# Kernel tuning notes

Hardware: AMD Instinct MI355X
Metric: run time of the kernel (lower is better)

Reference implementation:

```python
import jax, jax.numpy as jnp
import numpy as np

OUT_SIZE = 14
CUTOFF = 0.2
VAR0 = 4            # var[0], mixin_factor = 0.0 -> current std = var[0]
BETA = 4.0
N_SQ = OUT_SIZE * OUT_SIZE
TAU = 0.5 / N_SQ
BATCH = 256
CHANNELS = 512


def _gkern_np(kernlen, std, vmin, vmax):
    n = np.arange(kernlen) - (kernlen - 1) / 2.0
    w = np.exp(-(n ** 2) / (2.0 * std * std))
    g = np.outer(w, w)
    return g * (vmax - vmin) + vmin


def _build_templates():
    n = OUT_SIZE
    base = _gkern_np(2 * n - 1, VAR0, -CUTOFF, 1.0)
    base = np.maximum(base, 0.0) * 2.0 - 1.0
    base = TAU * np.clip(BETA * base / n, -1.0, None)  # clamp(min=-1) only
    # unfold(0,n,1).unfold(1,n,1).reshape(-1,n,n) == sliding windows, row-major
    t = np.lib.stride_tricks.sliding_window_view(base, (n, n)).reshape(-1, n, n)
    t = np.flip(t, axis=0).copy()  # torch.flip(templates, dims=(0,))
    templates_f = jnp.asarray(t, jnp.float32)                    # (n^2, n, n)
    neg = -TAU * jnp.ones((1, n, n), jnp.float32)
    templates_b = jnp.concatenate([templates_f, neg], axis=0)    # (n^2+1, n, n)
    alpha = N_SQ / (1.0 + N_SQ)
    p_T = jnp.asarray(
        np.array([alpha / N_SQ] * N_SQ + [1.0 - alpha], np.float32))  # (n^2+1,)
    return templates_f, templates_b, p_T


def setup_inputs() -> dict:
    key = jax.random.key(0)
    templates_f, templates_b, p_T = _build_templates()
    x = jax.random.normal(key, (BATCH, CHANNELS, OUT_SIZE, OUT_SIZE), jnp.float32)
    return {"x": x, "templates_f": templates_f,
            "templates_b": templates_b, "p_T": p_T}


def reference(x, templates_f, templates_b, p_T):
    B, C, H, W = x.shape
    tau = 0.5 / (H * W)
    # max_pool2d with kernel == full spatial extent -> flat argmax per (b, c)
    idx = jnp.argmax(x.reshape(B, C, H * W), axis=-1)            # (B, C) int
    sel = templates_f[idx]                                       # (B, C, H, W)
    mask = sel / jnp.max(sel)                                    # global max
    mask = jax.nn.relu(mask - CUTOFF) / CUTOFF
    x_masked = x * mask
    # local loss (mutual-information style) on the masked activations
    tr_x_T = jnp.einsum('bcwh,twh->cbt', x_masked * tau, templates_b)  # (C,B,T)
    p_x_T = jax.nn.softmax(tr_x_T, axis=1)                       # softmax over b
    p_x = jnp.einsum('t,cbt->cb', p_T, p_x_T)                    # (C, B)
    log_ratio = jnp.log(p_x_T / p_x[:, :, None])                 # (C, B, T)
    p_x_T_log = jnp.einsum('cbt,cbt->ct', p_x_T, log_ratio)      # (C, T)
    loss = -jnp.einsum('t,ct->c', p_T, p_x_T_log)                # (C,)
    return x_masked, mask, loss
```

## Files before the change

kernel.cpp:

```cpp
#include <hip/hip_runtime.h>

#define BB 256
#define CCH 512
#define HW 196
#define TT 197
#define TROWS 208
#define NFRAG (13 * 7)
#define ASHORTS (NFRAG * 64 * 8)
#define H1FRAG (7 * 7)
#define H2FRAG (6 * 7)
#define H1SHORTS (H1FRAG * 512)
#define H2SHORTS (H2FRAG * 512)

typedef __attribute__((ext_vector_type(8))) short bf16x8;
typedef __attribute__((ext_vector_type(4))) float f32x4;

__device__ __forceinline__ unsigned short f2bf(float f) {
    union { float f; unsigned u; } v; v.f = f;
    unsigned r = v.u + 0x7FFFu + ((v.u >> 16) & 1u);
    return (unsigned short)(r >> 16);
}

__global__ void prep(const float* __restrict__ tf, const float* __restrict__ tb,
                     float* __restrict__ wsf, unsigned short* __restrict__ tb_bf) {
    if (blockIdx.x < 182) {
        int i = blockIdx.x * 256 + threadIdx.x;
        int frag = i >> 9;
        int s    = i & 511;
        int mt = frag / 7, kt = frag % 7;
        int lane = s >> 3, j = s & 7;
        int r = mt * 16 + (lane & 15);
        int k = kt * 32 + (lane >> 4) * 8 + j;
        const float tau = 0.5f / 196.0f;
        float v = (r < TT && k < HW) ? tb[r * HW + k] * tau : 0.0f;
        tb_bf[i] = f2bf(v);
    } else {
        __shared__ float red[256];
        float m = -1e30f;
        for (int i = threadIdx.x; i < HW * HW; i += 256) m = fmaxf(m, tf[i]);
        red[threadIdx.x] = m;
        __syncthreads();
        for (int s = 128; s > 0; s >>= 1) {
            if (threadIdx.x < s) red[threadIdx.x] = fmaxf(red[threadIdx.x], red[threadIdx.x + s]);
            __syncthreads();
        }
        if (threadIdx.x == 0) wsf[0] = red[0];
    }
}

extern "C" __global__ __launch_bounds__(1024)
void fused_one(const float* __restrict__ x, const float* __restrict__ tf,
               const float* __restrict__ pT, const unsigned short* __restrict__ tb_bf,
               const float* __restrict__ wsf,
               float* __restrict__ xm_out, float* __restrict__ mask_out,
               float* __restrict__ loss_out)
{
    extern __shared__ char smem[];
    unsigned short* Alds = (unsigned short*)smem;
    float* s_part = (float*)(smem + H1SHORTS * 2);
    float* rAs    = s_part + 16 * TROWS;
    float* pTs    = rAs + TROWS;
    float* red    = pTs + TROWS;

    const int c    = blockIdx.x;
    const int tid  = threadIdx.x;
    const int lane = tid & 63;
    const int w    = tid >> 6;
    const int l15  = lane & 15, lg = lane >> 4;
    const float rg = 1.0f / wsf[0];

    {
        const f32x4* src = (const f32x4*)tb_bf;
        f32x4* dst = (f32x4*)Alds;
        #pragma unroll
        for (int it = 0; it < 4; ++it) {
            int idx = tid + it * 1024;
            if (idx < H1SHORTS / 8) dst[idx] = src[idx];
        }
    }
    if (tid < TROWS) pTs[tid] = (tid < TT) ? pT[tid] : 0.0f;

    const int b = w * 16 + l15;
    const size_t rowoff = ((size_t)b * CCH + c) * HW;
    const float* xrow = x + rowoff;

    f32x4 u[13];
    #pragma unroll
    for (int kt = 0; kt < 6; ++kt) {
        u[2 * kt]     = *(const f32x4*)(xrow + kt * 32 + lg * 8);
        u[2 * kt + 1] = *(const f32x4*)(xrow + kt * 32 + lg * 8 + 4);
    }
    if (lg == 0) u[12] = *(const f32x4*)(xrow + 192);
    else         u[12] = (f32x4){-__builtin_inff(), -__builtin_inff(),
                                 -__builtin_inff(), -__builtin_inff()};

    float bv = -__builtin_inff(); int bi = 0;
    #pragma unroll
    for (int j = 0; j < 13; ++j) {
        const int k0 = (j < 12) ? (((j >> 1) * 8 + lg * 2 + (j & 1)) * 4) : 192;
        #pragma unroll
        for (int e = 0; e < 4; ++e) {
            float v = u[j][e];
            if (v > bv) { bv = v; bi = k0 + e; }
        }
    }
    #pragma unroll
    for (int m = 16; m <= 32; m <<= 1) {
        float ov = __shfl_xor(bv, m, 64);
        int   oi = __shfl_xor(bi, m, 64);
        if (ov > bv || (ov == bv && oi < bi)) { bv = ov; bi = oi; }
    }

    const float* selrow = tf + (size_t)bi * HW;
    float* xmrow = xm_out + rowoff;
    float* mkrow = mask_out + rowoff;
    bf16x8 fr[7];

    #pragma unroll
    for (int kt = 0; kt < 6; ++kt) {
        #pragma unroll
        for (int h = 0; h < 2; ++h) {
            const int k0 = kt * 32 + lg * 8 + h * 4;
            f32x4 sel = *(const f32x4*)(selrow + k0);
            f32x4 mk, xm;
            #pragma unroll
            for (int e = 0; e < 4; ++e) {
                float m = fmaxf(sel[e] * rg - 0.2f, 0.0f) * 5.0f;
                mk[e] = m;
                xm[e] = u[2 * kt + h][e] * m;
            }
            *(f32x4*)(xmrow + k0) = xm;
            *(f32x4*)(mkrow + k0) = mk;
            #pragma unroll
            for (int e = 0; e < 4; ++e) fr[kt][h * 4 + e] = (short)f2bf(xm[e]);
        }
    }
    {
        fr[6] = (bf16x8){0, 0, 0, 0, 0, 0, 0, 0};
        if (lg == 0) {
            f32x4 sel = *(const f32x4*)(selrow + 192);
            f32x4 mk, xm;
            #pragma unroll
            for (int e = 0; e < 4; ++e) {
                float m = fmaxf(sel[e] * rg - 0.2f, 0.0f) * 5.0f;
                mk[e] = m;
                xm[e] = u[12][e] * m;
            }
            *(f32x4*)(xmrow + 192) = xm;
            *(f32x4*)(mkrow + 192) = mk;
            #pragma unroll
            for (int e = 0; e < 4; ++e) fr[6][e] = (short)f2bf(xm[e]);
        }
    }

    __syncthreads();

    f32x4 acc[13];
    #pragma unroll
    for (int mt = 0; mt < 13; ++mt) acc[mt] = (f32x4){0.f, 0.f, 0.f, 0.f};

    const unsigned short* Abase = Alds + lane * 8;
    #pragma unroll
    for (int kt = 0; kt < 7; ++kt) {
        const bf16x8 bfrag = fr[kt];
        #pragma unroll
        for (int mt = 0; mt < 7; ++mt) {
            bf16x8 afrag = *(const bf16x8*)(Abase + (mt * 7 + kt) * 512);
            acc[mt] = __builtin_amdgcn_mfma_f32_16x16x32_bf16(afrag, bfrag, acc[mt], 0, 0, 0);
        }
    }

    __syncthreads();

    {
        const f32x4* src = (const f32x4*)(tb_bf + H1SHORTS);
        f32x4* dst = (f32x4*)Alds;
        #pragma unroll
        for (int it = 0; it < 3; ++it) {
            int idx = tid + it * 1024;
            if (idx < H2SHORTS / 8) dst[idx] = src[idx];
        }
    }
    __syncthreads();

    #pragma unroll
    for (int kt = 0; kt < 7; ++kt) {
        const bf16x8 bfrag = fr[kt];
        #pragma unroll
        for (int mt = 7; mt < 13; ++mt) {
            bf16x8 afrag = *(const bf16x8*)(Abase + ((mt - 7) * 7 + kt) * 512);
            acc[mt] = __builtin_amdgcn_mfma_f32_16x16x32_bf16(afrag, bfrag, acc[mt], 0, 0, 0);
        }
    }

    float* sp = s_part + w * TROWS;
    #pragma unroll
    for (int mt = 0; mt < 13; ++mt) {
        #pragma unroll
        for (int e = 0; e < 4; ++e) acc[mt][e] = __expf(acc[mt][e]);
        f32x4 s = acc[mt];
        #pragma unroll
        for (int m = 1; m <= 8; m <<= 1) {
            #pragma unroll
            for (int e = 0; e < 4; ++e) s[e] += __shfl_xor(s[e], m, 64);
        }
        if (l15 == 0) *(f32x4*)(sp + mt * 16 + lg * 4) = s;
    }
    __syncthreads();
    if (tid < TROWS) {
        float s = 0.f;
        #pragma unroll
        for (int w2 = 0; w2 < 16; ++w2) s += s_part[w2 * TROWS + tid];
        rAs[tid] = 1.0f / s;
    }
    __syncthreads();

    float px = 0.f;
    #pragma unroll
    for (int mt = 0; mt < 13; ++mt) {
        const int t0 = mt * 16 + lg * 4;
        f32x4 ra = *(const f32x4*)(rAs + t0);
        f32x4 pt = *(const f32x4*)(pTs + t0);
        #pragma unroll
        for (int e = 0; e < 4; ++e) {
            float p = acc[mt][e] * ra[e];
            acc[mt][e] = p;
            px += pt[e] * p;
        }
    }
    px += __shfl_xor(px, 16, 64);
    px += __shfl_xor(px, 32, 64);
    const float rpx = 1.0f / px;

    float part = 0.f;
    #pragma unroll
    for (int mt = 0; mt < 13; ++mt) {
        const int t0 = mt * 16 + lg * 4;
        f32x4 pt = *(const f32x4*)(pTs + t0);
        #pragma unroll
        for (int e = 0; e < 4; ++e) {
            float p = acc[mt][e];
            part += pt[e] * p * __logf(p * rpx);
        }
    }
    #pragma unroll
    for (int off = 32; off >= 1; off >>= 1) part += __shfl_xor(part, off, 64);
    if (lane == 0) red[w] = part;
    __syncthreads();
    if (tid == 0) {
        float s = 0.f;
        #pragma unroll
        for (int w2 = 0; w2 < 16; ++w2) s += red[w2];
        loss_out[c] = -s;
    }
}

extern "C" void kernel_launch(void* const* d_in, const int* in_sizes, int n_in,
                              void* d_out, int out_size, void* d_ws, size_t ws_size,
                              hipStream_t stream) {
    const float* x  = (const float*)d_in[0];
    const float* tf = (const float*)d_in[1];
    const float* tb = (const float*)d_in[2];
    const float* pT = (const float*)d_in[3];

    const size_t NOUT = (size_t)BB * CCH * HW;
    float* xm_out = (float*)d_out;
    float* mk_out = xm_out + NOUT;
    float* ls_out = mk_out + NOUT;

    float* wsf = (float*)d_ws;
    unsigned short* tb_bf = (unsigned short*)((char*)d_ws + 64);

    prep<<<183, 256, 0, stream>>>(tf, tb, wsf, tb_bf);

    const size_t SMEM = (size_t)H1SHORTS * 2
                      + 16 * TROWS * 4
                      + TROWS * 4 + TROWS * 4 + 16 * 4;
    hipFuncSetAttribute((const void*)fused_one, hipFuncAttributeMaxDynamicSharedMemorySize, (int)SMEM);
    fused_one<<<dim3(CCH), dim3(1024), SMEM, stream>>>(x, tf, pT, tb_bf, wsf,
                                                       xm_out, mk_out, ls_out);
}
```

Before: 144.2 us.

## Split per-channel fused kernel into batch-quarter blocks with workspace-staged softmax reduction

Replaces the one-block-per-channel 1024-thread kernel with 2048 blocks of 256 threads. Each block handles a quarter of the batch for one channel, loads the templates into shared memory in smaller chunks, and writes the bf16 logits and partial column exp-sums to workspace. A second kernel combines the partial sums, computes the loss contributions, and a small third kernel finishes the per-channel sum. The aim is better occupancy and lower shared-memory pressure. In exchange it adds about 54MB of extra global traffic for the staged logits and two extra kernel launches. The old fused kernel is kept as a fallback when the workspace is too small.

```diff
diff --git a/kernel.cpp b/kernel.cpp
--- a/kernel.cpp
+++ b/kernel.cpp
@@ -7,22 +7,27 @@
 #define TROWS 208
 #define NFRAG (13 * 7)
 #define ASHORTS (NFRAG * 64 * 8)
-#define H1FRAG (7 * 7)
-#define H2FRAG (6 * 7)
-#define H1SHORTS (H1FRAG * 512)
-#define H2SHORTS (H2FRAG * 512)
+#define CST (CCH * TROWS)
+#define QMAX_SHORTS (4 * 7 * 512)
 
 typedef __attribute__((ext_vector_type(8))) short bf16x8;
 typedef __attribute__((ext_vector_type(4))) float f32x4;
+typedef __attribute__((ext_vector_type(4))) unsigned short us4;
 
 __device__ __forceinline__ unsigned short f2bf(float f) {
     union { float f; unsigned u; } v; v.f = f;
     unsigned r = v.u + 0x7FFFu + ((v.u >> 16) & 1u);
     return (unsigned short)(r >> 16);
 }
+__device__ __forceinline__ float bf2f(unsigned short h) {
+    union { unsigned u; float f; } v; v.u = ((unsigned)h) << 16;
+    return v.f;
+}
 
 __global__ void prep(const float* __restrict__ tf, const float* __restrict__ tb,
-                     float* __restrict__ wsf, unsigned short* __restrict__ tb_bf) {
+                     const float* __restrict__ pT,
+                     float* __restrict__ wsf, unsigned short* __restrict__ tb_bf,
+                     float* __restrict__ pT_pad) {
     if (blockIdx.x < 182) {
         int i = blockIdx.x * 256 + threadIdx.x;
         int frag = i >> 9;
@@ -35,6 +40,8 @@
         float v = (r < TT && k < HW) ? tb[r * HW + k] * tau : 0.0f;
         tb_bf[i] = f2bf(v);
     } else {
+        if (threadIdx.x < TROWS)
+            pT_pad[threadIdx.x] = (threadIdx.x < TT) ? pT[threadIdx.x] : 0.0f;
         __shared__ float red[256];
         float m = -1e30f;
         for (int i = threadIdx.x; i < HW * HW; i += 256) m = fmaxf(m, tf[i]);
@@ -48,12 +55,237 @@
     }
 }
 
+extern "C" __global__ __launch_bounds__(256)
+__attribute__((amdgpu_waves_per_eu(4, 4)))
+void k1_main(const float* __restrict__ x, const float* __restrict__ tf,
+             const unsigned short* __restrict__ tb_bf, const float* __restrict__ wsf,
+             float* __restrict__ xm_out, float* __restrict__ mask_out,
+             float* __restrict__ colp, unsigned short* __restrict__ trs)
+{
+    __shared__ unsigned short Alds[QMAX_SHORTS];
+    __shared__ float s_col[4][TROWS];
+
+    const int tid  = threadIdx.x;
+    const int lane = tid & 63;
+    const int w    = tid >> 6;
+    const int l15  = lane & 15, lg = lane >> 4;
+    const int c    = blockIdx.x >> 2, g = blockIdx.x & 3;
+    const float rg = 1.0f / wsf[0];
+
+    {
+        const f32x4* src = (const f32x4*)tb_bf;
+        f32x4* dst = (f32x4*)Alds;
+        #pragma unroll
+        for (int it = 0; it < 7; ++it) dst[tid + it * 256] = src[tid + it * 256];
+    }
+
+    const int b = g * 64 + w * 16 + l15;
+    const size_t rowoff = ((size_t)b * CCH + c) * HW;
+    const float* xrow = x + rowoff;
+
+    f32x4 u[13];
+    #pragma unroll
+    for (int kt = 0; kt < 6; ++kt) {
+        u[2 * kt]     = *(const f32x4*)(xrow + kt * 32 + lg * 8);
+        u[2 * kt + 1] = *(const f32x4*)(xrow + kt * 32 + lg * 8 + 4);
+    }
+    if (lg == 0) u[12] = *(const f32x4*)(xrow + 192);
+    else         u[12] = (f32x4){-__builtin_inff(), -__builtin_inff(),
+                                 -__builtin_inff(), -__builtin_inff()};
+
+    float bv = -__builtin_inff(); int bi = 0;
+    #pragma unroll
+    for (int j = 0; j < 13; ++j) {
+        const int k0 = (j < 12) ? (((j >> 1) * 8 + lg * 2 + (j & 1)) * 4) : 192;
+        #pragma unroll
+        for (int e = 0; e < 4; ++e) {
+            float v = u[j][e];
+            if (v > bv) { bv = v; bi = k0 + e; }
+        }
+    }
+    #pragma unroll
+    for (int m = 16; m <= 32; m <<= 1) {
+        float ov = __shfl_xor(bv, m, 64);
+        int   oi = __shfl_xor(bi, m, 64);
+        if (ov > bv || (ov == bv && oi < bi)) { bv = ov; bi = oi; }
+    }
+
+    const float* selrow = tf + (size_t)bi * HW;
+    float* xmrow = xm_out + rowoff;
+    float* mkrow = mask_out + rowoff;
+    bf16x8 fr[7];
+
+    #pragma unroll
+    for (int kt = 0; kt < 6; ++kt) {
+        #pragma unroll
+        for (int h = 0; h < 2; ++h) {
+            const int k0 = kt * 32 + lg * 8 + h * 4;
+            f32x4 sel = *(const f32x4*)(selrow + k0);
+            f32x4 mk, xm;
+            #pragma unroll
+            for (int e = 0; e < 4; ++e) {
+                float m = fmaxf(sel[e] * rg - 0.2f, 0.0f) * 5.0f;
+                mk[e] = m;
+                xm[e] = u[2 * kt + h][e] * m;
+            }
+            *(f32x4*)(xmrow + k0) = xm;
+            *(f32x4*)(mkrow + k0) = mk;
+            #pragma unroll
+            for (int e = 0; e < 4; ++e) fr[kt][h * 4 + e] = (short)f2bf(xm[e]);
+        }
+    }
+    {
+        fr[6] = (bf16x8){0, 0, 0, 0, 0, 0, 0, 0};
+        if (lg == 0) {
+            f32x4 sel = *(const f32x4*)(selrow + 192);
+            f32x4 mk, xm;
+            #pragma unroll
+            for (int e = 0; e < 4; ++e) {
+                float m = fmaxf(sel[e] * rg - 0.2f, 0.0f) * 5.0f;
+                mk[e] = m;
+                xm[e] = u[12][e] * m;
+            }
+            *(f32x4*)(xmrow + 192) = xm;
+            *(f32x4*)(mkrow + 192) = mk;
+            #pragma unroll
+            for (int e = 0; e < 4; ++e) fr[6][e] = (short)f2bf(xm[e]);
+        }
+    }
+
+    f32x4 acc[13];
+    #pragma unroll
+    for (int mt = 0; mt < 13; ++mt) acc[mt] = (f32x4){0.f, 0.f, 0.f, 0.f};
+
+    const unsigned short* Abase = Alds + lane * 8;
+
+    __syncthreads();
+    #pragma unroll
+    for (int mt = 0; mt < 4; ++mt) {
+        #pragma unroll
+        for (int kt = 0; kt < 7; ++kt)
+            acc[mt] = __builtin_amdgcn_mfma_f32_16x16x32_bf16(
+                *(const bf16x8*)(Abase + (mt * 7 + kt) * 512), fr[kt], acc[mt], 0, 0, 0);
+    }
+    __syncthreads();
+
+    #pragma unroll
+    for (int q = 1; q < 4; ++q) {
+        const int m0 = 4 + (q - 1) * 3;
+        {
+            const f32x4* src = (const f32x4*)tb_bf + m0 * 7 * 64;
+            f32x4* dst = (f32x4*)Alds;
+            #pragma unroll
+            for (int it = 0; it < 6; ++it) {
+                int idx = tid + it * 256;
+                if (idx < 1344) dst[idx] = src[idx];
+            }
+        }
+        __syncthreads();
+        #pragma unroll
+        for (int mi = 0; mi < 3; ++mi) {
+            const int mt = m0 + mi;
+            #pragma unroll
+            for (int kt = 0; kt < 7; ++kt)
+                acc[mt] = __builtin_amdgcn_mfma_f32_16x16x32_bf16(
+                    *(const bf16x8*)(Abase + (mi * 7 + kt) * 512), fr[kt], acc[mt], 0, 0, 0);
+        }
+        __syncthreads();
+    }
+
+    unsigned short* trow = trs + (((size_t)c * 4 + g) * 64 + w * 16 + l15) * TROWS;
+    #pragma unroll
+    for (int mt = 0; mt < 13; ++mt) {
+        us4 pk;
+        #pragma unroll
+        for (int e = 0; e < 4; ++e) pk[e] = f2bf(acc[mt][e]);
+        *(us4*)(trow + mt * 16 + lg * 4) = pk;
+
+        f32x4 s;
+        #pragma unroll
+        for (int e = 0; e < 4; ++e) s[e] = __expf(acc[mt][e]);
+        #pragma unroll
+        for (int m = 1; m <= 8; m <<= 1) {
+            #pragma unroll
+            for (int e = 0; e < 4; ++e) s[e] += __shfl_xor(s[e], m, 64);
+        }
+        if (l15 == 0) *(f32x4*)(&s_col[w][mt * 16 + lg * 4]) = s;
+    }
+    __syncthreads();
+    if (tid < TROWS) {
+        float s = s_col[0][tid] + s_col[1][tid] + s_col[2][tid] + s_col[3][tid];
+        colp[(size_t)g * CST + c * TROWS + tid] = s;
+    }
+}
+
+extern "C" __global__ __launch_bounds__(256)
+void k2_loss(const unsigned short* __restrict__ trs, const float* __restrict__ pT_pad,
+             const float* __restrict__ colp, float* __restrict__ loss_part)
+{
+    __shared__ float rAs[TROWS];
+    __shared__ float lAs[TROWS];
+    __shared__ float pTs[TROWS];
+    __shared__ float red[4];
+
+    const int tid  = threadIdx.x;
+    const int lane = tid & 63;
+    const int w    = tid >> 6;
+    const int c    = blockIdx.x >> 2, g = blockIdx.x & 3;
+
+    if (tid < TROWS) {
+        const float* cpc = colp + (size_t)c * TROWS + tid;
+        float A = cpc[0] + cpc[CST] + cpc[2 * CST] + cpc[3 * CST];
+        rAs[tid] = 1.0f / A;
+        lAs[tid] = __logf(A);
+        pTs[tid] = pT_pad[tid];
+    }
+    __syncthreads();
+
+    const int p4 = tid & 3;
+    const unsigned short* trow = trs + (((size_t)c * 4 + g) * 64 + (tid >> 2)) * TROWS;
+
+    float px = 0.f, S1 = 0.f;
+    #pragma unroll
+    for (int j = 0; j < 13; ++j) {
+        const int t0 = (p4 + 4 * j) * 4;
+        us4 tv = *(const us4*)(trow + t0);
+        #pragma unroll
+        for (int e = 0; e < 4; ++e) {
+            const int t = t0 + e;
+            float tr = bf2f(tv[e]);
+            float p  = __expf(tr) * rAs[t];
+            px += pTs[t] * p;
+            S1 += pTs[t] * p * (tr - lAs[t]);
+        }
+    }
+    px += __shfl_xor(px, 1, 64);
+    px += __shfl_xor(px, 2, 64);
+    S1 += __shfl_xor(S1, 1, 64);
+    S1 += __shfl_xor(S1, 2, 64);
+    float part = (p4 == 0) ? (S1 - px * __logf(px)) : 0.0f;
+    #pragma unroll
+    for (int off = 4; off <= 32; off <<= 1) part += __shfl_xor(part, off, 64);
+    if (lane == 0) red[w] = part;
+    __syncthreads();
+    if (tid == 0) loss_part[(size_t)c * 4 + g] = red[0] + red[1] + red[2] + red[3];
+}
+
+__global__ void k3_fin(const float* __restrict__ lp, float* __restrict__ loss_out) {
+    int c = blockIdx.x * 256 + threadIdx.x;
+    if (c < CCH)
+        loss_out[c] = -(lp[4 * c] + lp[4 * c + 1] + lp[4 * c + 2] + lp[4 * c + 3]);
+}
+
+#define H1FRAG (7 * 7)
+#define H2FRAG (6 * 7)
+#define H1SHORTS (H1FRAG * 512)
+#define H2SHORTS (H2FRAG * 512)
+
 extern "C" __global__ __launch_bounds__(1024)
-void fused_one(const float* __restrict__ x, const float* __restrict__ tf,
-               const float* __restrict__ pT, const unsigned short* __restrict__ tb_bf,
-               const float* __restrict__ wsf,
-               float* __restrict__ xm_out, float* __restrict__ mask_out,
-               float* __restrict__ loss_out)
+void fused_fb(const float* __restrict__ x, const float* __restrict__ tf,
+              const float* __restrict__ pT, const unsigned short* __restrict__ tb_bf,
+              const float* __restrict__ wsf,
+              float* __restrict__ xm_out, float* __restrict__ mask_out,
+              float* __restrict__ loss_out)
 {
     extern __shared__ char smem[];
     unsigned short* Alds = (unsigned short*)smem;
@@ -164,14 +396,11 @@
     for (int kt = 0; kt < 7; ++kt) {
         const bf16x8 bfrag = fr[kt];
         #pragma unroll
-        for (int mt = 0; mt < 7; ++mt) {
-            bf16x8 afrag = *(const bf16x8*)(Abase + (mt * 7 + kt) * 512);
-            acc[mt] = __builtin_amdgcn_mfma_f32_16x16x32_bf16(afrag, bfrag, acc[mt], 0, 0, 0);
-        }
-    }
-
-    __syncthreads();
-
+        for (int mt = 0; mt < 7; ++mt)
+            acc[mt] = __builtin_amdgcn_mfma_f32_16x16x32_bf16(
+                *(const bf16x8*)(Abase + (mt * 7 + kt) * 512), bfrag, acc[mt], 0, 0, 0);
+    }
+    __syncthreads();
     {
         const f32x4* src = (const f32x4*)(tb_bf + H1SHORTS);
         f32x4* dst = (f32x4*)Alds;
@@ -182,15 +411,13 @@
         }
     }
     __syncthreads();
-
     #pragma unroll
     for (int kt = 0; kt < 7; ++kt) {
         const bf16x8 bfrag = fr[kt];
         #pragma unroll
-        for (int mt = 7; mt < 13; ++mt) {
-            bf16x8 afrag = *(const bf16x8*)(Abase + ((mt - 7) * 7 + kt) * 512);
-            acc[mt] = __builtin_amdgcn_mfma_f32_16x16x32_bf16(afrag, bfrag, acc[mt], 0, 0, 0);
-        }
+        for (int mt = 7; mt < 13; ++mt)
+            acc[mt] = __builtin_amdgcn_mfma_f32_16x16x32_bf16(
+                *(const bf16x8*)(Abase + ((mt - 7) * 7 + kt) * 512), bfrag, acc[mt], 0, 0, 0);
     }
 
     float* sp = s_part + w * TROWS;
@@ -268,15 +495,27 @@
     float* mk_out = xm_out + NOUT;
     float* ls_out = mk_out + NOUT;
 
-    float* wsf = (float*)d_ws;
-    unsigned short* tb_bf = (unsigned short*)((char*)d_ws + 64);
-
-    prep<<<183, 256, 0, stream>>>(tf, tb, wsf, tb_bf);
-
-    const size_t SMEM = (size_t)H1SHORTS * 2
-                      + 16 * TROWS * 4
-                      + TROWS * 4 + TROWS * 4 + 16 * 4;
-    hipFuncSetAttribute((const void*)fused_one, hipFuncAttributeMaxDynamicSharedMemorySize, (int)SMEM);
-    fused_one<<<dim3(CCH), dim3(1024), SMEM, stream>>>(x, tf, pT, tb_bf, wsf,
-                                                       xm_out, mk_out, ls_out);
-}
+    char* wsp = (char*)d_ws;
+    float*          wsf    = (float*)wsp;
+    unsigned short* tb_bf  = (unsigned short*)(wsp + 64);
+    float*          pT_pad = (float*)(wsp + 93312);
+    float*          colp   = (float*)(wsp + 94208);
+    float*          lpart  = (float*)(wsp + 1798144);
+    unsigned short* trs    = (unsigned short*)(wsp + 1806336);
+    const bool big = ws_size >= (size_t)1806336 + 54525952;
+
+    prep<<<183, 256, 0, stream>>>(tf, tb, pT, wsf, tb_bf, pT_pad);
+
+    if (big) {
+        k1_main<<<2048, 256, 0, stream>>>(x, tf, tb_bf, wsf, xm_out, mk_out, colp, trs);
+        k2_loss<<<2048, 256, 0, stream>>>(trs, pT_pad, colp, lpart);
+        k3_fin<<<2, 256, 0, stream>>>(lpart, ls_out);
+    } else {
+        const size_t SMEM = (size_t)H1SHORTS * 2 + 16 * TROWS * 4
+                          + 2 * TROWS * 4 + 16 * 4;
+        (void)hipFuncSetAttribute((const void*)fused_fb,
+                                  hipFuncAttributeMaxDynamicSharedMemorySize, (int)SMEM);
+        fused_fb<<<dim3(CCH), dim3(1024), SMEM, stream>>>(x, tf, pT, tb_bf, wsf,
+                                                          xm_out, mk_out, ls_out);
+    }
+}
```

Result: slower. 168.1 us (+16.5%).
